# Kernel optimization log

Hardware: AMD Instinct MI355X
Metric: run time of the kernel (lower is better)

Reference implementation:

```python
import jax, jax.numpy as jnp
import numpy as np

EPS = 1e-8  # torch F.cosine_similarity eps


def setup_inputs() -> dict:
    key = jax.random.key(0)
    k1, k2 = jax.random.split(key)
    z = jax.random.normal(k1, (32768, 2048), dtype=jnp.float32)
    expert_keys = jax.random.normal(k2, (64, 2048), dtype=jnp.float32)
    return {"z": z, "expert_keys": expert_keys}


def reference(z, expert_keys):
    # cosine similarity: (z . ek) / max(||z||*||ek||, eps)  -> [N, E]
    dots = jnp.einsum("nd,ed->ne", z, expert_keys)
    z_norm = jnp.linalg.norm(z, axis=-1)            # [N]
    e_norm = jnp.linalg.norm(expert_keys, axis=-1)  # [E]
    similarity = dots / jnp.maximum(z_norm[:, None] * e_norm[None, :], EPS)
    # softmax over experts, then weighted combination of expert keys -> [N, D]
    weighted_expert = jax.nn.softmax(similarity, axis=-1) @ expert_keys
    return similarity, weighted_expert
```

## Files before the change

kernel.cpp:

```cpp
#include <hip/hip_runtime.h>
#include <hip/hip_bf16.h>

typedef __attribute__((ext_vector_type(4))) float f32x4;
typedef __attribute__((ext_vector_type(8))) short bf16x8;

#define NROWS 32768
#define DIM   2048
#define NEXP  64
#define BKF   128
#define NCH   (DIM / BKF)

__device__ __forceinline__ short f2bf(float f) {
    __hip_bfloat16 h = __float2bfloat16(f);
    short s;
    __builtin_memcpy(&s, &h, 2);
    return s;
}

__device__ __forceinline__ void async16(const void* g, void* l) {
    __builtin_amdgcn_global_load_lds(
        (const __attribute__((address_space(1))) unsigned int*)g,
        (__attribute__((address_space(3))) unsigned int*)l, 16, 0, 0);
}

__global__ __launch_bounds__(256) void prep_experts(
    const float* __restrict__ ek,
    short* __restrict__ ekbf,
    short* __restrict__ ekT,
    float* __restrict__ enorm)
{
    const int e = blockIdx.x;
    const int t = threadIdx.x;
    const float* row = ek + e * DIM;
    float ss = 0.f;
#pragma unroll
    for (int i = 0; i < 2; ++i) {
        const int c4 = t + i * 256;
        const float4 v = ((const float4*)row)[c4];
        ss += v.x * v.x + v.y * v.y + v.z * v.z + v.w * v.w;
        short4 b;
        b.x = f2bf(v.x); b.y = f2bf(v.y); b.z = f2bf(v.z); b.w = f2bf(v.w);
        *(short4*)(ekbf + e * DIM + c4 * 4) = b;
        const int d = c4 * 4;
        ekT[(d + 0) * NEXP + e] = b.x;
        ekT[(d + 1) * NEXP + e] = b.y;
        ekT[(d + 2) * NEXP + e] = b.z;
        ekT[(d + 3) * NEXP + e] = b.w;
    }
#pragma unroll
    for (int s = 1; s < 64; s <<= 1) ss += __shfl_xor(ss, s);
    __shared__ float red[4];
    if ((t & 63) == 0) red[t >> 6] = ss;
    __syncthreads();
    if (t == 0) enorm[e] = sqrtf(red[0] + red[1] + red[2] + red[3]);
}

__global__ __launch_bounds__(256) void sim_kernel(
    const float* __restrict__ z,
    const short* __restrict__ ekbf,
    const float* __restrict__ enorm,
    float* __restrict__ out_sim)
{
    const int tid = threadIdx.x;
    const int w   = tid >> 6;
    const int l   = tid & 63;
    const int lr  = l & 15;
    const int lg  = l >> 4;
    const int base = blockIdx.x * 32;

    __shared__ __align__(16) float zbuf[2][32][BKF];
    __shared__ __align__(16) short ebuf[2][64][BKF];

    f32x4 acc[2];
    acc[0] = f32x4{0.f, 0.f, 0.f, 0.f};
    acc[1] = f32x4{0.f, 0.f, 0.f, 0.f};
    float sqa[2] = {0.f, 0.f}, sqb[2] = {0.f, 0.f};

    auto STAGE = [&](int c_) {
        const int b_ = c_ & 1;
#pragma unroll
        for (int i = 0; i < 4; ++i) {
            const int r0 = w * 8 + i * 2;
            const int zr = r0 + (l >> 5);
            async16(z + (size_t)(base + zr) * DIM + c_ * BKF
                      + (((l & 31) ^ (zr & 7)) << 2),
                    &zbuf[b_][r0][0]);
        }
#pragma unroll
        for (int i = 0; i < 4; ++i) {
            const int r0 = w * 16 + i * 4;
            const int er = r0 + (l >> 4);
            async16(ekbf + (size_t)er * DIM + c_ * BKF
                         + (((l & 15) ^ (er & 7)) << 3),
                    &ebuf[b_][r0][0]);
        }
    };

    STAGE(0); STAGE(1);

    for (int c = 0; c < NCH; ++c) {
        if (c < NCH - 1) asm volatile("s_waitcnt vmcnt(8)" ::: "memory");
        else             asm volatile("s_waitcnt vmcnt(0)" ::: "memory");
        __builtin_amdgcn_s_barrier();
        __builtin_amdgcn_sched_barrier(0);
        const int b = c & 1;

#pragma unroll
        for (int kk = 0; kk < BKF / 32; ++kk) {
            const int eu = ((kk * 4 + lg) ^ (lr & 7)) << 4;
            const bf16x8 bf =
                *(const bf16x8*)((const char*)&ebuf[b][w * 16 + lr][0] + eu);
#pragma unroll
            for (int mt = 0; mt < 2; ++mt) {
                const int zr = mt * 16 + lr;
                const int u0 = ((kk * 8 + lg * 2)     ^ (lr & 7)) << 4;
                const int u1 = ((kk * 8 + lg * 2 + 1) ^ (lr & 7)) << 4;
                const float4 a0 = *(const float4*)((const char*)&zbuf[b][zr][0] + u0);
                const float4 a1 = *(const float4*)((const char*)&zbuf[b][zr][0] + u1);
                sqa[mt] = fmaf(a0.x, a0.x, sqa[mt]); sqb[mt] = fmaf(a0.y, a0.y, sqb[mt]);
                sqa[mt] = fmaf(a0.z, a0.z, sqa[mt]); sqb[mt] = fmaf(a0.w, a0.w, sqb[mt]);
                sqa[mt] = fmaf(a1.x, a1.x, sqa[mt]); sqb[mt] = fmaf(a1.y, a1.y, sqb[mt]);
                sqa[mt] = fmaf(a1.z, a1.z, sqa[mt]); sqb[mt] = fmaf(a1.w, a1.w, sqb[mt]);
                bf16x8 af;
                af[0] = f2bf(a0.x); af[1] = f2bf(a0.y); af[2] = f2bf(a0.z); af[3] = f2bf(a0.w);
                af[4] = f2bf(a1.x); af[5] = f2bf(a1.y); af[6] = f2bf(a1.z); af[7] = f2bf(a1.w);
                acc[mt] = __builtin_amdgcn_mfma_f32_16x16x32_bf16(af, bf, acc[mt], 0, 0, 0);
            }
        }
        __builtin_amdgcn_s_barrier();
        if (c + 2 < NCH) STAGE(c + 2);
    }

    const float en = enorm[w * 16 + lr];
#pragma unroll
    for (int mt = 0; mt < 2; ++mt) {
        float ss = sqa[mt] + sqb[mt];
        ss += __shfl_xor(ss, 16);
        ss += __shfl_xor(ss, 32);
        const float zn = sqrtf(ss);
#pragma unroll
        for (int j = 0; j < 4; ++j) {
            const float znj = __shfl(zn, lg * 4 + j);
            out_sim[(size_t)(base + mt * 16 + lg * 4 + j) * NEXP + w * 16 + lr]
                = acc[mt][j] / fmaxf(znj * en, 1e-8f);
        }
    }
}

__global__ __launch_bounds__(256) void moe_kernel(
    const float* __restrict__ sim,
    const short* __restrict__ ekT,
    float* __restrict__ out_wei)
{
    const int tid = threadIdx.x;
    const int w   = tid >> 6;
    const int l   = tid & 63;
    const int lr  = l & 15;
    const int lg  = l >> 4;
    const int base = blockIdx.x * 32;
    const int col0 = blockIdx.y * 1024;

    __shared__ __align__(16) short WL[32][64];
    __shared__ __align__(16) float tbuf[32][260];

    {
        const int r  = tid >> 3;
        const int cc = tid & 7;
        const float* sp = sim + (size_t)(base + r) * NEXP + cc * 8;
        const float4 v0 = *(const float4*)sp;
        const float4 v1 = *(const float4*)(sp + 4);
        float va[8] = {v0.x, v0.y, v0.z, v0.w, v1.x, v1.y, v1.z, v1.w};
        float m = va[0];
#pragma unroll
        for (int i = 1; i < 8; ++i) m = fmaxf(m, va[i]);
        m = fmaxf(m, __shfl_xor(m, 1));
        m = fmaxf(m, __shfl_xor(m, 2));
        m = fmaxf(m, __shfl_xor(m, 4));
        float sum = 0.f;
#pragma unroll
        for (int i = 0; i < 8; ++i) { va[i] = __expf(va[i] - m); sum += va[i]; }
        sum += __shfl_xor(sum, 1);
        sum += __shfl_xor(sum, 2);
        sum += __shfl_xor(sum, 4);
        const float inv = 1.0f / sum;
        bf16x8 wv;
#pragma unroll
        for (int i = 0; i < 8; ++i) wv[i] = f2bf(va[i] * inv);
        *(bf16x8*)&WL[r][(cc ^ (r & 7)) * 8] = wv;
    }
    __syncthreads();

    bf16x8 afr[2][2];
#pragma unroll
    for (int mt = 0; mt < 2; ++mt)
#pragma unroll
        for (int ks = 0; ks < 2; ++ks) {
            const int row = mt * 16 + lr;
            const int u   = (ks * 4 + lg) ^ (row & 7);
            afr[mt][ks] = *(const bf16x8*)&WL[row][u * 8];
        }

#pragma unroll 1
    for (int g = 0; g < 4; ++g) {
        f32x4 oacc[4][2];
#pragma unroll
        for (int nt2 = 0; nt2 < 4; ++nt2) {
            const int d0 = col0 + g * 256 + w * 64 + nt2 * 16;
            const short* bp = ekT + (size_t)(d0 + lr) * NEXP + lg * 8;
            const bf16x8 b0 = *(const bf16x8*)bp;
            const bf16x8 b1 = *(const bf16x8*)(bp + 32);
#pragma unroll
            for (int mt = 0; mt < 2; ++mt) {
                f32x4 o = f32x4{0.f, 0.f, 0.f, 0.f};
                o = __builtin_amdgcn_mfma_f32_16x16x32_bf16(afr[mt][0], b0, o, 0, 0, 0);
                o = __builtin_amdgcn_mfma_f32_16x16x32_bf16(afr[mt][1], b1, o, 0, 0, 0);
                oacc[nt2][mt] = o;
            }
        }
#pragma unroll
        for (int nt2 = 0; nt2 < 4; ++nt2)
#pragma unroll
            for (int mt = 0; mt < 2; ++mt)
#pragma unroll
                for (int j = 0; j < 4; ++j)
                    tbuf[mt * 16 + lg * 4 + j][w * 64 + nt2 * 16 + lr] = oacc[nt2][mt][j];
        __syncthreads();
#pragma unroll
        for (int i = 0; i < 8; ++i) {
            const int row = w * 8 + i;
            const float4 t = *(const float4*)&tbuf[row][l * 4];
            *(float4*)&out_wei[(size_t)(base + row) * DIM + col0 + g * 256 + l * 4] = t;
        }
        __syncthreads();
    }
}

extern "C" void kernel_launch(void* const* d_in, const int* in_sizes, int n_in,
                              void* d_out, int out_size, void* d_ws, size_t ws_size,
                              hipStream_t stream) {
    const float* z  = (const float*)d_in[0];
    const float* ek = (const float*)d_in[1];
    float* out_sim = (float*)d_out;
    float* out_wei = out_sim + (size_t)NROWS * NEXP;

    short* ekbf  = (short*)d_ws;
    short* ekT   = ekbf + NEXP * DIM;
    float* enorm = (float*)(ekT + DIM * NEXP);

    prep_experts<<<NEXP, 256, 0, stream>>>(ek, ekbf, ekT, enorm);
    sim_kernel<<<NROWS / 32, 256, 0, stream>>>(z, ekbf, enorm, out_sim);
    moe_kernel<<<dim3(NROWS / 32, 2), 256, 0, stream>>>(out_sim, ekT, out_wei);
}
```

Measured before the change: 150.6 us.

## Deepen z prefetch pipeline and read expert keys directly from global

The similarity kernel now processes 16 rows per block with 256-wide K chunks, and keeps four LDS slots for z with three chunks in flight. The expert-key bf16 tile is no longer staged through LDS; each lane reads its B fragment straight from global/L2. One barrier per chunk replaces two. The aim is to hide more HBM latency on the dominant z stream and to cut LDS traffic and synchronisation. The risk is that the in-loop global loads for expert keys share the vmcnt counter with the async z loads. Compiler-inserted waits for those loads may stall the pipeline, and each expert-key tile is now re-read by twice as many blocks.

```diff
diff --git a/kernel.cpp b/kernel.cpp
--- a/kernel.cpp
+++ b/kernel.cpp
@@ -7,7 +7,7 @@
 #define NROWS 32768
 #define DIM   2048
 #define NEXP  64
-#define BKF   128
+#define BKF   256
 #define NCH   (DIM / BKF)
 
 __device__ __forceinline__ short f2bf(float f) {
@@ -66,84 +66,66 @@
     const int l   = tid & 63;
     const int lr  = l & 15;
     const int lg  = l >> 4;
-    const int base = blockIdx.x * 32;
-
-    __shared__ __align__(16) float zbuf[2][32][BKF];
-    __shared__ __align__(16) short ebuf[2][64][BKF];
-
-    f32x4 acc[2];
-    acc[0] = f32x4{0.f, 0.f, 0.f, 0.f};
-    acc[1] = f32x4{0.f, 0.f, 0.f, 0.f};
-    float sqa[2] = {0.f, 0.f}, sqb[2] = {0.f, 0.f};
-
-    auto STAGE = [&](int c_) {
-        const int b_ = c_ & 1;
+    const int base = blockIdx.x * 16;
+
+    __shared__ __align__(16) float zbuf[4][16][BKF];
+
+    f32x4 acc = f32x4{0.f, 0.f, 0.f, 0.f};
+    float ss0 = 0.f, ss1 = 0.f;
+
+    auto STAGE_Z = [&](int c_, int slot) {
 #pragma unroll
         for (int i = 0; i < 4; ++i) {
-            const int r0 = w * 8 + i * 2;
-            const int zr = r0 + (l >> 5);
+            const int zr = w * 4 + i;
             async16(z + (size_t)(base + zr) * DIM + c_ * BKF
-                      + (((l & 31) ^ (zr & 7)) << 2),
-                    &zbuf[b_][r0][0]);
-        }
-#pragma unroll
-        for (int i = 0; i < 4; ++i) {
-            const int r0 = w * 16 + i * 4;
-            const int er = r0 + (l >> 4);
-            async16(ekbf + (size_t)er * DIM + c_ * BKF
-                         + (((l & 15) ^ (er & 7)) << 3),
-                    &ebuf[b_][r0][0]);
+                      + (((l ^ (zr & 7)) & 63) << 2),
+                    &zbuf[slot][zr][0]);
         }
     };
 
-    STAGE(0); STAGE(1);
+    STAGE_Z(0, 0); STAGE_Z(1, 1); STAGE_Z(2, 2);
+
+    const short* ebase = ekbf + (size_t)(w * 16 + lr) * DIM + lg * 8;
 
     for (int c = 0; c < NCH; ++c) {
-        if (c < NCH - 1) asm volatile("s_waitcnt vmcnt(8)" ::: "memory");
-        else             asm volatile("s_waitcnt vmcnt(0)" ::: "memory");
+        if (c < NCH - 2)       asm volatile("s_waitcnt vmcnt(8)" ::: "memory");
+        else if (c == NCH - 2) asm volatile("s_waitcnt vmcnt(4)" ::: "memory");
+        else                   asm volatile("s_waitcnt vmcnt(0)" ::: "memory");
         __builtin_amdgcn_s_barrier();
         __builtin_amdgcn_sched_barrier(0);
-        const int b = c & 1;
-
+        if (c + 3 < NCH) STAGE_Z(c + 3, (c + 3) & 3);
+
+        const int zs = c & 3;
 #pragma unroll
         for (int kk = 0; kk < BKF / 32; ++kk) {
-            const int eu = ((kk * 4 + lg) ^ (lr & 7)) << 4;
-            const bf16x8 bf =
-                *(const bf16x8*)((const char*)&ebuf[b][w * 16 + lr][0] + eu);
-#pragma unroll
-            for (int mt = 0; mt < 2; ++mt) {
-                const int zr = mt * 16 + lr;
-                const int u0 = ((kk * 8 + lg * 2)     ^ (lr & 7)) << 4;
-                const int u1 = ((kk * 8 + lg * 2 + 1) ^ (lr & 7)) << 4;
-                const float4 a0 = *(const float4*)((const char*)&zbuf[b][zr][0] + u0);
-                const float4 a1 = *(const float4*)((const char*)&zbuf[b][zr][0] + u1);
-                sqa[mt] = fmaf(a0.x, a0.x, sqa[mt]); sqb[mt] = fmaf(a0.y, a0.y, sqb[mt]);
-                sqa[mt] = fmaf(a0.z, a0.z, sqa[mt]); sqb[mt] = fmaf(a0.w, a0.w, sqb[mt]);
-                sqa[mt] = fmaf(a1.x, a1.x, sqa[mt]); sqb[mt] = fmaf(a1.y, a1.y, sqb[mt]);
-                sqa[mt] = fmaf(a1.z, a1.z, sqa[mt]); sqb[mt] = fmaf(a1.w, a1.w, sqb[mt]);
-                bf16x8 af;
-                af[0] = f2bf(a0.x); af[1] = f2bf(a0.y); af[2] = f2bf(a0.z); af[3] = f2bf(a0.w);
-                af[4] = f2bf(a1.x); af[5] = f2bf(a1.y); af[6] = f2bf(a1.z); af[7] = f2bf(a1.w);
-                acc[mt] = __builtin_amdgcn_mfma_f32_16x16x32_bf16(af, bf, acc[mt], 0, 0, 0);
-            }
-        }
-        __builtin_amdgcn_s_barrier();
-        if (c + 2 < NCH) STAGE(c + 2);
-    }
+            const bf16x8 bf = *(const bf16x8*)(ebase + c * BKF + kk * 32);
+            const int u0 = ((kk * 8 + lg * 2)     ^ (lr & 7)) << 4;
+            const int u1 = ((kk * 8 + lg * 2 + 1) ^ (lr & 7)) << 4;
+            const char* zrowp = (const char*)&zbuf[zs][lr][0];
+            const float4 a0 = *(const float4*)(zrowp + u0);
+            const float4 a1 = *(const float4*)(zrowp + u1);
+            ss0 = fmaf(a0.x, a0.x, ss0); ss1 = fmaf(a0.y, a0.y, ss1);
+            ss0 = fmaf(a0.z, a0.z, ss0); ss1 = fmaf(a0.w, a0.w, ss1);
+            ss0 = fmaf(a1.x, a1.x, ss0); ss1 = fmaf(a1.y, a1.y, ss1);
+            ss0 = fmaf(a1.z, a1.z, ss0); ss1 = fmaf(a1.w, a1.w, ss1);
+            bf16x8 af;
+            af[0] = f2bf(a0.x); af[1] = f2bf(a0.y); af[2] = f2bf(a0.z); af[3] = f2bf(a0.w);
+            af[4] = f2bf(a1.x); af[5] = f2bf(a1.y); af[6] = f2bf(a1.z); af[7] = f2bf(a1.w);
+            acc = __builtin_amdgcn_mfma_f32_16x16x32_bf16(af, bf, acc, 0, 0, 0);
+        }
+    }
+
+    float ssq = ss0 + ss1;
+    ssq += __shfl_xor(ssq, 16);
+    ssq += __shfl_xor(ssq, 32);
+    const float zn = sqrtf(ssq);
 
     const float en = enorm[w * 16 + lr];
 #pragma unroll
-    for (int mt = 0; mt < 2; ++mt) {
-        float ss = sqa[mt] + sqb[mt];
-        ss += __shfl_xor(ss, 16);
-        ss += __shfl_xor(ss, 32);
-        const float zn = sqrtf(ss);
-#pragma unroll
-        for (int j = 0; j < 4; ++j) {
-            const float znj = __shfl(zn, lg * 4 + j);
-            out_sim[(size_t)(base + mt * 16 + lg * 4 + j) * NEXP + w * 16 + lr]
-                = acc[mt][j] / fmaxf(znj * en, 1e-8f);
-        }
+    for (int j = 0; j < 4; ++j) {
+        const float znj = __shfl(zn, lg * 4 + j);
+        out_sim[(size_t)(base + lg * 4 + j) * NEXP + w * 16 + lr]
+            = acc[j] / fmaxf(znj * en, 1e-8f);
     }
 }
 
@@ -248,6 +230,6 @@
     float* enorm = (float*)(ekT + DIM * NEXP);
 
     prep_experts<<<NEXP, 256, 0, stream>>>(ek, ekbf, ekT, enorm);
-    sim_kernel<<<NROWS / 32, 256, 0, stream>>>(z, ekbf, enorm, out_sim);
+    sim_kernel<<<NROWS / 16, 256, 0, stream>>>(z, ekbf, enorm, out_sim);
     moe_kernel<<<dim3(NROWS / 32, 2), 256, 0, stream>>>(out_sim, ekT, out_wei);
 }
```

Measured after the change: 167.2 us. 11.0% more time.
